# Optimization experiments

Hardware: AMD Instinct MI355X
Metric: run time of the kernel (lower is better)

The kernel has to match this reference:

```python
import jax, jax.numpy as jnp
import numpy as np

NUM_NODES = 50000
NUM_EDGES = 800000
IN_C = 64
OUT_C = 64


def setup_inputs() -> dict:
    key = jax.random.key(0)
    k1, k2, k3, k4 = jax.random.split(key, 4)
    x = jax.random.normal(k1, (NUM_NODES, IN_C), dtype=jnp.float32)
    edge_index = jax.random.randint(k2, (2, NUM_EDGES), 0, NUM_NODES, dtype=jnp.int64)
    # nn.Linear params (kaiming-uniform-ish init scale)
    lim = 1.0 / np.sqrt(IN_C)
    W = jax.random.uniform(k3, (OUT_C, IN_C), minval=-lim, maxval=lim, dtype=jnp.float32)
    b = jax.random.uniform(k4, (OUT_C,), minval=-lim, maxval=lim, dtype=jnp.float32)
    return {"x": x, "edge_index": edge_index, "W": W, "b": b}


def reference(x, edge_index, W, b):
    num_nodes = x.shape[0]
    src = edge_index[0]
    tgt = edge_index[1]
    # Stage 1: degree of target nodes via scatter-add of ones
    deg = jax.ops.segment_sum(jnp.ones(src.shape[0], dtype=jnp.float32), tgt,
                              num_segments=num_nodes)
    deg_inv_sqrt = jnp.clip(deg, 1.0, None) ** -0.5  # [N]
    # Stage 2-3: gather source features, scale by norm_src * norm_tgt
    norm = deg_inv_sqrt[src] * deg_inv_sqrt[tgt]       # [E]
    messages = x[src] * norm[:, None]                  # [E, C]
    # Stage 4: scatter-add aggregation into target nodes
    agg = jax.ops.segment_sum(messages, tgt, num_segments=num_nodes)  # [N, C]
    # Stage 5-6: linear + relu
    out = agg @ W.T + b
    return jax.nn.relu(out)
```

## Files before the change

kernel.cpp:

```cpp
#include <hip/hip_runtime.h>
#include <hip/hip_fp16.h>

#define NN 50000
#define NE 800000
#define NE4 (NE / 4)
#define NC 64
#define CAP 64
#define NXCD 8
#define NODES_PER (NN / NXCD)
#define BIN_BLOCKS 2048
#define BIN_STRIDE ((BIN_BLOCKS / NXCD) * 256)

__global__ void FusedGCN_zero_kernel(int4* __restrict__ p, int n4) {
    int t = blockIdx.x * blockDim.x + threadIdx.x;
    if (t < n4) p[t] = make_int4(0, 0, 0, 0);
}


__global__ __launch_bounds__(256) void FusedGCN_binA2_kernel(
        const int4* __restrict__ src4,
        const int4* __restrict__ tgt4,
        int* __restrict__ counters,
        int* __restrict__ binned) {
    int grp = blockIdx.x & (NXCD - 1);
    int sub = blockIdx.x >> 3;
    int lo = grp * NODES_PER, hi = lo + NODES_PER;

    int i0 = sub * 256 + threadIdx.x;
    int i1 = i0 + BIN_STRIDE;
    int i2 = i1 + BIN_STRIDE;
    int i3 = i2 + BIN_STRIDE;

    const int4 none = make_int4(-1, -1, -1, -1);
    int4 t0 = (i0 < NE4) ? tgt4[i0] : none;
    int4 t1 = (i1 < NE4) ? tgt4[i1] : none;
    int4 t2 = (i2 < NE4) ? tgt4[i2] : none;
    int4 t3 = (i3 < NE4) ? tgt4[i3] : none;
    int4 s0 = (i0 < NE4) ? src4[i0] : none;
    int4 s1 = (i1 < NE4) ? src4[i1] : none;
    int4 s2 = (i2 < NE4) ? src4[i2] : none;
    int4 s3 = (i3 < NE4) ? src4[i3] : none;

#define PROC(T, S)                                                       \
    if ((T) >= lo && (T) < hi) {                                         \
        int p_ = atomicAdd(&counters[(T)], 1);                           \
        if (p_ < CAP) binned[((T) << 6) + p_] = (S);                     \
    }
    PROC(t0.x, s0.x) PROC(t0.y, s0.y) PROC(t0.z, s0.z) PROC(t0.w, s0.w)
    PROC(t1.x, s1.x) PROC(t1.y, s1.y) PROC(t1.z, s1.z) PROC(t1.w, s1.w)
    PROC(t2.x, s2.x) PROC(t2.y, s2.y) PROC(t2.z, s2.z) PROC(t2.w, s2.w)
    PROC(t3.x, s3.x) PROC(t3.y, s3.y) PROC(t3.z, s3.z) PROC(t3.w, s3.w)
#undef PROC
}

__global__ void FusedGCN_xscaleH_kernel(const float4* __restrict__ x4,
                                        const int* __restrict__ counters,
                                        uint2* __restrict__ xsh2) {
    int t = blockIdx.x * blockDim.x + threadIdx.x;
    if (t < (NN + 1) * (NC / 4)) {
        int row = t >> 4;
        float4 v = make_float4(0.f, 0.f, 0.f, 0.f);
        if (row < NN) {
            float d = rsqrtf(fmaxf((float)counters[row], 1.0f));
            v = x4[t];
            v.x *= d; v.y *= d; v.z *= d; v.w *= d;
        }
        __half2 h0 = __floats2half2_rn(v.x, v.y);
        __half2 h1 = __floats2half2_rn(v.z, v.w);
        uint2 u;
        u.x = *(unsigned int*)&h0;
        u.y = *(unsigned int*)&h1;
        xsh2[t] = u;
    }
}

__global__ __launch_bounds__(256) void FusedGCN_aggA_kernel(
        const uint2* __restrict__ xs2,
        const int* __restrict__ binned,
        const int* __restrict__ counters,
        const float* __restrict__ W,
        const float4* __restrict__ bias4,
        float4* __restrict__ out4) {
    __shared__ float Wt[64][68];
    int tid = threadIdx.x;
    for (int i = tid; i < 64 * 64; i += 256) Wt[i & 63][i >> 6] = W[i];
    __syncthreads();

    int lane = tid & 63;
    int g    = lane >> 4;
    int gl   = lane & 15;
    int base = g << 4;
    int node = (blockIdx.x << 4) + ((tid >> 6) << 2) + g;

    int cnt = min(counters[node], CAP);
    int4 sv = ((const int4*)binned)[(node << 4) + gl];
    int k0 = gl << 2;
    int s0 = (k0 + 0 < cnt) ? sv.x : NN;
    int s1 = (k0 + 1 < cnt) ? sv.y : NN;
    int s2 = (k0 + 2 < cnt) ? sv.z : NN;
    int s3 = (k0 + 3 < cnt) ? sv.w : NN;

    float4 acc = make_float4(0.f, 0.f, 0.f, 0.f);

#define H4ACC(raw)                                                   \
    {                                                                \
        __half2 _h0 = *(__half2*)&(raw).x;                           \
        __half2 _h1 = *(__half2*)&(raw).y;                           \
        float2 _f0 = __half22float2(_h0);                            \
        float2 _f1 = __half22float2(_h1);                            \
        acc.x += _f0.x; acc.y += _f0.y;                              \
        acc.z += _f1.x; acc.w += _f1.y;                              \
    }

    for (int q = 0; q < 4; ++q) {
        if ((q << 4) >= cnt) break;
        int L = base + (q << 2);
        int a0 = __shfl(s0, L + 0), a1 = __shfl(s1, L + 0);
        int a2 = __shfl(s2, L + 0), a3 = __shfl(s3, L + 0);
        int b0 = __shfl(s0, L + 1), b1 = __shfl(s1, L + 1);
        int b2 = __shfl(s2, L + 1), b3 = __shfl(s3, L + 1);
        int c0 = __shfl(s0, L + 2), c1 = __shfl(s1, L + 2);
        int c2 = __shfl(s2, L + 2), c3 = __shfl(s3, L + 2);
        int d0 = __shfl(s0, L + 3), d1 = __shfl(s1, L + 3);
        int d2 = __shfl(s2, L + 3), d3 = __shfl(s3, L + 3);
        uint2 v0 = xs2[(a0 << 4) + gl], v1 = xs2[(a1 << 4) + gl];
        uint2 v2 = xs2[(a2 << 4) + gl], v3 = xs2[(a3 << 4) + gl];
        uint2 v4 = xs2[(b0 << 4) + gl], v5 = xs2[(b1 << 4) + gl];
        uint2 v6 = xs2[(b2 << 4) + gl], v7 = xs2[(b3 << 4) + gl];
        uint2 v8 = xs2[(c0 << 4) + gl], v9 = xs2[(c1 << 4) + gl];
        uint2 va = xs2[(c2 << 4) + gl], vb = xs2[(c3 << 4) + gl];
        uint2 vc = xs2[(d0 << 4) + gl], vd = xs2[(d1 << 4) + gl];
        uint2 ve = xs2[(d2 << 4) + gl], vf = xs2[(d3 << 4) + gl];
        H4ACC(v0) H4ACC(v1) H4ACC(v2) H4ACC(v3)
        H4ACC(v4) H4ACC(v5) H4ACC(v6) H4ACC(v7)
        H4ACC(v8) H4ACC(v9) H4ACC(va) H4ACC(vb)
        H4ACC(vc) H4ACC(vd) H4ACC(ve) H4ACC(vf)
    }
#undef H4ACC

    float dn = rsqrtf(fmaxf((float)cnt, 1.0f));
    acc.x *= dn; acc.y *= dn; acc.z *= dn; acc.w *= dn;

    float4 r = bias4[gl];
#pragma unroll
    for (int kk = 0; kk < 16; ++kk) {
        int sl = base + kk;
        float ax = __shfl(acc.x, sl);
        float ay = __shfl(acc.y, sl);
        float az = __shfl(acc.z, sl);
        float aw = __shfl(acc.w, sl);
        const float4 w0 = *(const float4*)&Wt[(kk << 2) + 0][gl << 2];
        const float4 w1 = *(const float4*)&Wt[(kk << 2) + 1][gl << 2];
        const float4 w2 = *(const float4*)&Wt[(kk << 2) + 2][gl << 2];
        const float4 w3 = *(const float4*)&Wt[(kk << 2) + 3][gl << 2];
        r.x = fmaf(ax, w0.x, fmaf(ay, w1.x, fmaf(az, w2.x, fmaf(aw, w3.x, r.x))));
        r.y = fmaf(ax, w0.y, fmaf(ay, w1.y, fmaf(az, w2.y, fmaf(aw, w3.y, r.y))));
        r.z = fmaf(ax, w0.z, fmaf(ay, w1.z, fmaf(az, w2.z, fmaf(aw, w3.z, r.z))));
        r.w = fmaf(ax, w0.w, fmaf(ay, w1.w, fmaf(az, w2.w, fmaf(aw, w3.w, r.w))));
    }
    r.x = fmaxf(r.x, 0.f); r.y = fmaxf(r.y, 0.f);
    r.z = fmaxf(r.z, 0.f); r.w = fmaxf(r.w, 0.f);
    out4[(node << 4) + gl] = r;
}

__global__ void FusedGCN_count_kernel(const int* __restrict__ tgt,
                                      int* __restrict__ counters) {
    int e = blockIdx.x * blockDim.x + threadIdx.x;
    if (e < NE) atomicAdd(&counters[tgt[e]], 1);
}

__global__ __launch_bounds__(256) void FusedGCN_alloc_kernel(
        const int* __restrict__ counters,
        int* __restrict__ gcursor,
        int* __restrict__ offsets,
        int* __restrict__ cursor,
        float* __restrict__ dis) {
    int i = blockIdx.x * blockDim.x + threadIdx.x;
    int lane = threadIdx.x & 63;
    int c = (i < NN) ? counters[i] : 0;
    int v = c;
#pragma unroll
    for (int o = 1; o < 64; o <<= 1) {
        int t = __shfl_up(v, o, 64);
        if (lane >= o) v += t;
    }
    int waveTotal = __shfl(v, 63, 64);
    int base = 0;
    if (lane == 63) base = atomicAdd(gcursor, waveTotal);
    base = __shfl(base, 63, 64);
    if (i < NN) {
        int start = base + v - c;
        offsets[i] = start;
        cursor[i]  = start;
        dis[i] = rsqrtf(fmaxf((float)c, 1.0f));
    }
}

__global__ void FusedGCN_bin_kernel(const int* __restrict__ src,
                                    const int* __restrict__ tgt,
                                    int* __restrict__ cursor,
                                    int* __restrict__ binned) {
    int e = blockIdx.x * blockDim.x + threadIdx.x;
    if (e < NE) {
        int pos = atomicAdd(&cursor[tgt[e]], 1);
        binned[pos] = src[e];
    }
}

__global__ __launch_bounds__(256) void FusedGCN_agg_kernel(
        const float* __restrict__ x,
        const int* __restrict__ binned,
        const int* __restrict__ offsets,
        const int* __restrict__ counters,
        const float* __restrict__ dis,
        const float* __restrict__ W,
        const float* __restrict__ bias,
        float* __restrict__ out) {
    __shared__ float Wt[64][65];
    int tid = threadIdx.x;
    for (int i = tid; i < 64 * 64; i += 256) Wt[i & 63][i >> 6] = W[i];
    __syncthreads();

    int lane = tid & 63;
    int node = blockIdx.x * 4 + (tid >> 6);
    if (node >= NN) return;

    int off = offsets[node];
    int end = off + counters[node];
    float acc = 0.0f;
    for (int c = off; c < end; c += 64) {
        int m = min(64, end - c);
        int   sidx = 0;
        float nv   = 0.0f;
        if (lane < m) {
            sidx = binned[c + lane];
            nv   = dis[sidx];
        }
        int j = 0;
        for (; j + 4 <= m; j += 4) {
            int   s0 = __shfl(sidx, j),     s1 = __shfl(sidx, j + 1);
            int   s2 = __shfl(sidx, j + 2), s3 = __shfl(sidx, j + 3);
            float n0 = __shfl(nv, j),       n1 = __shfl(nv, j + 1);
            float n2 = __shfl(nv, j + 2),   n3 = __shfl(nv, j + 3);
            acc = fmaf(x[s0 * NC + lane], n0, acc);
            acc = fmaf(x[s1 * NC + lane], n1, acc);
            acc = fmaf(x[s2 * NC + lane], n2, acc);
            acc = fmaf(x[s3 * NC + lane], n3, acc);
        }
        for (; j < m; ++j) {
            acc = fmaf(x[__shfl(sidx, j) * NC + lane], __shfl(nv, j), acc);
        }
    }
    acc *= dis[node];

    float r = bias[lane];
#pragma unroll
    for (int k = 0; k < 64; ++k) r = fmaf(__shfl(acc, k), Wt[k][lane], r);
    out[node * NC + lane] = fmaxf(r, 0.0f);
}

extern "C" void kernel_launch(void* const* d_in, const int* in_sizes, int n_in,
                              void* d_out, int out_size, void* d_ws, size_t ws_size,
                              hipStream_t stream) {
    const float* x   = (const float*)d_in[0];
    const int*   ei  = (const int*)d_in[1];
    const float* W   = (const float*)d_in[2];
    const float* b   = (const float*)d_in[3];
    const int*   src = ei;
    const int*   tgt = ei + NE;
    float* out = (float*)d_out;

    size_t off_binned = (size_t)NN * 4;
    size_t off_xs     = off_binned + (size_t)NN * CAP * 4;
    size_t needA      = off_xs + (size_t)(NN + 1) * NC * 2;

    if (ws_size >= needA) {
        int*   counters = (int*)d_ws;
        int*   binned   = (int*)((char*)d_ws + off_binned);
        uint2* xsh2     = (uint2*)((char*)d_ws + off_xs);

        FusedGCN_zero_kernel<<<(NN / 4 + 255) / 256, 256, 0, stream>>>(
            (int4*)counters, NN / 4);
        FusedGCN_binA2_kernel<<<BIN_BLOCKS, 256, 0, stream>>>(
            (const int4*)src, (const int4*)tgt, counters, binned);
        FusedGCN_xscaleH_kernel<<<((NN + 1) * (NC / 4) + 255) / 256, 256, 0, stream>>>(
            (const float4*)x, counters, xsh2);
        FusedGCN_aggA_kernel<<<NN / 16, 256, 0, stream>>>(
            xsh2, binned, counters, W, (const float4*)b, (float4*)out);
    } else {
        int*   counters = (int*)d_ws;
        int*   gcursor  = counters + NN;
        int*   offsets  = gcursor + 1;
        int*   cursor   = offsets + NN;
        float* dis      = (float*)(cursor + NN);
        int*   binned   = (int*)(dis + NN);

        FusedGCN_zero_kernel<<<(NN / 4 + 255) / 256, 256, 0, stream>>>(
            (int4*)counters, NN / 4);
        hipMemsetAsync(gcursor, 0, sizeof(int), stream);
        FusedGCN_count_kernel<<<(NE + 255) / 256, 256, 0, stream>>>(tgt, counters);
        FusedGCN_alloc_kernel<<<(NN + 255) / 256, 256, 0, stream>>>(
            counters, gcursor, offsets, cursor, dis);
        FusedGCN_bin_kernel<<<(NE + 255) / 256, 256, 0, stream>>>(
            src, tgt, cursor, binned);
        FusedGCN_agg_kernel<<<(NN + 3) / 4, 256, 0, stream>>>(
            x, binned, offsets, counters, dis, W, b, out);
    }
}
```

Baseline: 85.76 us.

## Replace global-atomic binning with LDS-counted slices and per-node prefix scan

Replaces the single binning kernel, which used global atomics on per-node counters, with three passes. The first pass counts targets per node in LDS for each of 64 edge slices. The second runs a per-node exclusive scan over the slice counts. The third bins source indices using LDS atomics plus the scanned base offsets. This removes contended global atomics and the separate zeroing kernel, at the cost of two extra launches, reading the edge list twice and a 6.4 MB count matrix. The edge order inside each bin also becomes deterministic per slice.

```diff
diff --git a/kernel.cpp b/kernel.cpp
--- a/kernel.cpp
+++ b/kernel.cpp
@@ -8,8 +8,8 @@
 #define CAP 64
 #define NXCD 8
 #define NODES_PER (NN / NXCD)
-#define BIN_BLOCKS 2048
-#define BIN_STRIDE ((BIN_BLOCKS / NXCD) * 256)
+#define SLICES 64
+#define EPS4 (NE4 / SLICES)
 
 __global__ void FusedGCN_zero_kernel(int4* __restrict__ p, int n4) {
     int t = blockIdx.x * blockDim.x + threadIdx.x;
@@ -17,40 +17,81 @@
 }
 
 
-__global__ __launch_bounds__(256) void FusedGCN_binA2_kernel(
+__global__ __launch_bounds__(256) void FusedGCN_p1_count(
+        const int4* __restrict__ tgt4,
+        unsigned short* __restrict__ cnt) {
+    __shared__ int lcnt[NODES_PER];
+    int g = blockIdx.x & (NXCD - 1);
+    int b = blockIdx.x >> 3;
+    int lo = g * NODES_PER;
+    for (int i = threadIdx.x; i < NODES_PER; i += 256) lcnt[i] = 0;
+    __syncthreads();
+    int i1 = (b + 1) * EPS4;
+    for (int i = b * EPS4 + threadIdx.x; i < i1; i += 256) {
+        int4 t4 = tgt4[i];
+        int a;
+        a = t4.x - lo; if ((unsigned)a < NODES_PER) atomicAdd(&lcnt[a], 1);
+        a = t4.y - lo; if ((unsigned)a < NODES_PER) atomicAdd(&lcnt[a], 1);
+        a = t4.z - lo; if ((unsigned)a < NODES_PER) atomicAdd(&lcnt[a], 1);
+        a = t4.w - lo; if ((unsigned)a < NODES_PER) atomicAdd(&lcnt[a], 1);
+    }
+    __syncthreads();
+    for (int i = threadIdx.x; i < NODES_PER; i += 256)
+        cnt[(size_t)(lo + i) * SLICES + b] = (unsigned short)lcnt[i];
+}
+
+__global__ __launch_bounds__(256) void FusedGCN_p2_scan(
+        unsigned int* __restrict__ cnt,
+        int* __restrict__ counters) {
+    int n = blockIdx.x * 256 + threadIdx.x;
+    if (n >= NN) return;
+    uint4* p = (uint4*)(cnt + (size_t)n * (SLICES / 2));
+    uint4 r0 = p[0], r1 = p[1], r2 = p[2], r3 = p[3];
+    uint4 r4 = p[4], r5 = p[5], r6 = p[6], r7 = p[7];
+    int run = 0;
+#define SC(u) { unsigned c0 = (u) & 0xffffu, c1 = (u) >> 16;              \
+                (u) = (unsigned)run | ((unsigned)(run + c0) << 16);        \
+                run += (int)(c0 + c1); }
+    SC(r0.x) SC(r0.y) SC(r0.z) SC(r0.w)
+    SC(r1.x) SC(r1.y) SC(r1.z) SC(r1.w)
+    SC(r2.x) SC(r2.y) SC(r2.z) SC(r2.w)
+    SC(r3.x) SC(r3.y) SC(r3.z) SC(r3.w)
+    SC(r4.x) SC(r4.y) SC(r4.z) SC(r4.w)
+    SC(r5.x) SC(r5.y) SC(r5.z) SC(r5.w)
+    SC(r6.x) SC(r6.y) SC(r6.z) SC(r6.w)
+    SC(r7.x) SC(r7.y) SC(r7.z) SC(r7.w)
+#undef SC
+    p[0] = r0; p[1] = r1; p[2] = r2; p[3] = r3;
+    p[4] = r4; p[5] = r5; p[6] = r6; p[7] = r7;
+    counters[n] = run;
+}
+
+__global__ __launch_bounds__(256) void FusedGCN_p3_bin(
         const int4* __restrict__ src4,
         const int4* __restrict__ tgt4,
-        int* __restrict__ counters,
+        const unsigned short* __restrict__ base,
         int* __restrict__ binned) {
-    int grp = blockIdx.x & (NXCD - 1);
-    int sub = blockIdx.x >> 3;
-    int lo = grp * NODES_PER, hi = lo + NODES_PER;
-
-    int i0 = sub * 256 + threadIdx.x;
-    int i1 = i0 + BIN_STRIDE;
-    int i2 = i1 + BIN_STRIDE;
-    int i3 = i2 + BIN_STRIDE;
-
-    const int4 none = make_int4(-1, -1, -1, -1);
-    int4 t0 = (i0 < NE4) ? tgt4[i0] : none;
-    int4 t1 = (i1 < NE4) ? tgt4[i1] : none;
-    int4 t2 = (i2 < NE4) ? tgt4[i2] : none;
-    int4 t3 = (i3 < NE4) ? tgt4[i3] : none;
-    int4 s0 = (i0 < NE4) ? src4[i0] : none;
-    int4 s1 = (i1 < NE4) ? src4[i1] : none;
-    int4 s2 = (i2 < NE4) ? src4[i2] : none;
-    int4 s3 = (i3 < NE4) ? src4[i3] : none;
-
-#define PROC(T, S)                                                       \
-    if ((T) >= lo && (T) < hi) {                                         \
-        int p_ = atomicAdd(&counters[(T)], 1);                           \
-        if (p_ < CAP) binned[((T) << 6) + p_] = (S);                     \
-    }
-    PROC(t0.x, s0.x) PROC(t0.y, s0.y) PROC(t0.z, s0.z) PROC(t0.w, s0.w)
-    PROC(t1.x, s1.x) PROC(t1.y, s1.y) PROC(t1.z, s1.z) PROC(t1.w, s1.w)
-    PROC(t2.x, s2.x) PROC(t2.y, s2.y) PROC(t2.z, s2.z) PROC(t2.w, s2.w)
-    PROC(t3.x, s3.x) PROC(t3.y, s3.y) PROC(t3.z, s3.z) PROC(t3.w, s3.w)
-#undef PROC
+    __shared__ int lcnt[NODES_PER];
+    int g = blockIdx.x & (NXCD - 1);
+    int b = blockIdx.x >> 3;
+    int lo = g * NODES_PER;
+    for (int i = threadIdx.x; i < NODES_PER; i += 256) lcnt[i] = 0;
+    __syncthreads();
+    int i1 = (b + 1) * EPS4;
+    for (int i = b * EPS4 + threadIdx.x; i < i1; i += 256) {
+        int4 t4 = tgt4[i];
+        int4 s4 = src4[i];
+        int a;
+#define B1(T, S)                                                          \
+        a = (T) - lo;                                                     \
+        if ((unsigned)a < NODES_PER) {                                    \
+            int pl = atomicAdd(&lcnt[a], 1);                              \
+            int pos = (int)base[(size_t)(T) * SLICES + b] + pl;           \
+            if (pos < CAP) binned[((T) << 6) + pos] = (S);                \
+        }
+        B1(t4.x, s4.x) B1(t4.y, s4.y) B1(t4.z, s4.z) B1(t4.w, s4.w)
+#undef B1
+    }
 }
 
 __global__ void FusedGCN_xscaleH_kernel(const float4* __restrict__ x4,
@@ -272,17 +313,21 @@
 
     size_t off_binned = (size_t)NN * 4;
     size_t off_xs     = off_binned + (size_t)NN * CAP * 4;
-    size_t needA      = off_xs + (size_t)(NN + 1) * NC * 2;
+    size_t off_cnt    = off_xs + (size_t)(NN + 1) * NC * 2;
+    size_t needA      = off_cnt + (size_t)NN * SLICES * 2;
 
     if (ws_size >= needA) {
-        int*   counters = (int*)d_ws;
-        int*   binned   = (int*)((char*)d_ws + off_binned);
-        uint2* xsh2     = (uint2*)((char*)d_ws + off_xs);
-
-        FusedGCN_zero_kernel<<<(NN / 4 + 255) / 256, 256, 0, stream>>>(
-            (int4*)counters, NN / 4);
-        FusedGCN_binA2_kernel<<<BIN_BLOCKS, 256, 0, stream>>>(
-            (const int4*)src, (const int4*)tgt, counters, binned);
+        int*            counters = (int*)d_ws;
+        int*            binned   = (int*)((char*)d_ws + off_binned);
+        uint2*          xsh2     = (uint2*)((char*)d_ws + off_xs);
+        unsigned short* cnt      = (unsigned short*)((char*)d_ws + off_cnt);
+
+        FusedGCN_p1_count<<<NXCD * SLICES, 256, 0, stream>>>(
+            (const int4*)tgt, cnt);
+        FusedGCN_p2_scan<<<(NN + 255) / 256, 256, 0, stream>>>(
+            (unsigned int*)cnt, counters);
+        FusedGCN_p3_bin<<<NXCD * SLICES, 256, 0, stream>>>(
+            (const int4*)src, (const int4*)tgt, cnt, binned);
         FusedGCN_xscaleH_kernel<<<((NN + 1) * (NC / 4) + 255) / 256, 256, 0, stream>>>(
             (const float4*)x, counters, xsh2);
         FusedGCN_aggA_kernel<<<NN / 16, 256, 0, stream>>>(
```

After: 90.40 us. 5.4% more time.
